# Kernel optimization log

Hardware: AMD Instinct MI355X
Metric: run time of the kernel (lower is better)

The kernel has to match this reference:

```python
import jax, jax.numpy as jnp
import numpy as np

EPS = 1e-5  # torch GroupNorm default eps


def _pairwise_sqdist(x, y):
    # squared euclidean distance matrix, clamped at 0 for numerical safety
    d = (jnp.sum(x * x, -1)[:, None] + jnp.sum(y * y, -1)[None, :]
         - 2.0 * (x @ y.T))
    return jnp.maximum(d, 0.0)


def _pc_normalize(ref, src):
    # jointly center and scale both clouds to the unit sphere
    pts = jnp.concatenate([ref, src], axis=0)
    centroid = pts.mean(axis=0, keepdims=True)
    pts = pts - centroid
    m = jnp.max(jnp.linalg.norm(pts, axis=1))
    pts = pts / m
    n_ref = ref.shape[0]
    return pts[:n_ref], pts[n_ref:]


def _group_norm(x, gamma, beta, groups):
    N, C = x.shape
    xg = x.reshape(N, groups, C // groups)
    mean = xg.mean(-1, keepdims=True)
    var = jnp.mean((xg - mean) ** 2, -1, keepdims=True)
    xn = ((xg - mean) / jnp.sqrt(var + EPS)).reshape(N, C)
    return xn * gamma + beta


def setup_inputs() -> dict:
    key = jax.random.key(0)
    ks = jax.random.split(key, 8)
    N_ref, N_src, D = 128, 128, 256
    points_c = jax.random.normal(ks[0], (N_ref + N_src, 3), jnp.float32)
    ref_feats = jax.random.normal(ks[1], (N_ref, D), jnp.float32)
    src_feats = jax.random.normal(ks[2], (N_src, D), jnp.float32)
    # normalized features, as the '_norm' names suggest
    ref_feats = ref_feats / jnp.linalg.norm(ref_feats, axis=-1, keepdims=True)
    src_feats = src_feats / jnp.linalg.norm(src_feats, axis=-1, keepdims=True)
    # a valid rigid transform: random rotation + small translation
    A = jax.random.normal(ks[3], (3, 3), jnp.float32)
    Q, _ = jnp.linalg.qr(A)
    trans = jnp.eye(4, dtype=jnp.float32)
    trans = trans.at[:3, :3].set(Q)
    trans = trans.at[:3, 3].set(jax.random.normal(ks[4], (3,), jnp.float32) * 0.1)
    s = 1.0 / np.sqrt(512)
    return {
        'points_c': points_c,
        'ref_feats_c_norm': ref_feats,
        'src_feats_c_norm': src_feats,
        'trans': trans,
        'W1': jax.random.normal(ks[5], (256, 512), jnp.float32) * s,
        'b1': jnp.zeros((256,), jnp.float32),
        'g1': jnp.ones((256,), jnp.float32),
        'bt1': jnp.zeros((256,), jnp.float32),
        'W2': jax.random.normal(ks[6], (128, 256), jnp.float32) * (1.0 / np.sqrt(256)),
        'b2': jnp.zeros((128,), jnp.float32),
        'g2': jnp.ones((128,), jnp.float32),
        'bt2': jnp.zeros((128,), jnp.float32),
        'W3': jax.random.normal(ks[7], (2, 128), jnp.float32) * (1.0 / np.sqrt(128)),
        'b3': jnp.zeros((2,), jnp.float32),
        'ref_length': 128,
    }


def reference(points_c, ref_feats_c_norm, src_feats_c_norm, trans,
              W1, b1, g1, bt1, W2, b2, g2, bt2, W3, b3, ref_length):
    GROUPS = 8
    ref_points = points_c[:ref_length]
    src_points = points_c[ref_length:]
    # apply rigid transform to src points
    src_points = src_points @ trans[:3, :3].T + trans[:3, 3]
    ref_n, src_n = _pc_normalize(ref_points, src_points)

    dist_mat = jnp.exp(-_pairwise_sqdist(ref_n, src_n))  # [Nr, Ns]
    match_idx_ref = jnp.argmax(dist_mat, axis=1)
    match_idx_src = jnp.argmax(dist_mat, axis=0)
    min_dist_ref = jnp.max(dist_mat, axis=1)
    min_dist_src = jnp.max(dist_mat, axis=0)

    feat_score_mat = ref_feats_c_norm @ src_feats_c_norm.T  # [Nr, Ns]
    feat_match_idx_ref = jnp.argmax(feat_score_mat, axis=1)
    feat_match_idx_src = jnp.argmax(feat_score_mat, axis=0)
    feat_match_ref = jnp.max(feat_score_mat, axis=1)
    feat_match_src = jnp.max(feat_score_mat, axis=0)

    r_idx = jnp.arange(feat_score_mat.shape[0])
    c_idx = jnp.arange(feat_score_mat.shape[1])
    feat_score_ref = feat_score_mat[r_idx, match_idx_ref]
    feat_score_src = feat_score_mat[match_idx_src, c_idx]
    dist_ref = dist_mat[r_idx, feat_match_idx_ref]
    dist_src = dist_mat[feat_match_idx_src, c_idx]

    min_dist = jnp.concatenate([min_dist_ref, min_dist_src])
    feat_score = jnp.concatenate([feat_score_ref, feat_score_src])
    perm_d = jnp.argsort(-min_dist)  # descending sort
    d_m = min_dist[perm_d] * feat_score[perm_d]

    match_feat = jnp.concatenate([feat_match_ref, feat_match_src])
    match_dist = jnp.concatenate([dist_ref, dist_src])
    perm_f = jnp.argsort(-match_feat)
    m_d = match_dist[perm_f] * match_feat[perm_f]

    geo_out = jnp.concatenate([d_m, m_d])[None, :]  # [1, 512]

    h = _group_norm(geo_out @ W1.T + b1, g1, bt1, GROUPS)
    h = jax.nn.relu(h)
    h = _group_norm(h @ W2.T + b2, g2, bt2, GROUPS)
    h = jax.nn.relu(h)
    return h @ W3.T + b3  # [1, num_classes]
```

## Files before the change

kernel.cpp:

```cpp
#include <hip/hip_runtime.h>
#include <math.h>

#define NREF 128
#define NSRC 128
#define DIM  256
#define EPS  1e-5f

__global__ __launch_bounds__(512) void feat_kernel(
    const float* __restrict__ ref_feats,
    const float* __restrict__ src_feats,
    const float* __restrict__ points_c,
    const float* __restrict__ trans,
    float* __restrict__ feat_mat,
    float* __restrict__ rowF, int* __restrict__ rowFi,
    float* __restrict__ pts_ws)
{
    __shared__ __align__(16) float refrow[DIM];
    __shared__ float wmv[8];  __shared__ int wmi[8];
    __shared__ float wred[16], red[4];

    const int t = threadIdx.x;
    const int w = t >> 6, l = t & 63;

    if (blockIdx.x == 128) {
        float x = 0.f, y = 0.f, z = 0.f;
        if (t < 256) {
            x = points_c[3 * t + 0];
            y = points_c[3 * t + 1];
            z = points_c[3 * t + 2];
            if (t >= NREF) {
                float nx = trans[0] * x + trans[1] * y + trans[2]  * z + trans[3];
                float ny = trans[4] * x + trans[5] * y + trans[6]  * z + trans[7];
                float nz = trans[8] * x + trans[9] * y + trans[10] * z + trans[11];
                x = nx; y = ny; z = nz;
            }
            float sx = x, sy = y, sz = z;
            for (int off = 32; off >= 1; off >>= 1) {
                sx += __shfl_down(sx, off);
                sy += __shfl_down(sy, off);
                sz += __shfl_down(sz, off);
            }
            if (l == 0) {
                wred[w] = sx; wred[4 + w] = sy; wred[8 + w] = sz;
            }
        }
        __syncthreads();
        if (t == 0) {
            red[0] = (wred[0] + wred[1] + wred[2] + wred[3]) * (1.0f / 256.0f);
            red[1] = (wred[4] + wred[5] + wred[6] + wred[7]) * (1.0f / 256.0f);
            red[2] = (wred[8] + wred[9] + wred[10] + wred[11]) * (1.0f / 256.0f);
        }
        __syncthreads();
        if (t < 256) {
            x -= red[0]; y -= red[1]; z -= red[2];
            float n = x * x + y * y + z * z;
            float mx = n;
            for (int off = 32; off >= 1; off >>= 1)
                mx = fmaxf(mx, __shfl_down(mx, off));
            if (l == 0) wred[w] = mx;
        }
        __syncthreads();
        if (t == 0)
            red[3] = 1.0f / sqrtf(fmaxf(fmaxf(wred[0], wred[1]), fmaxf(wred[2], wred[3])));
        __syncthreads();
        if (t < 256) {
            const float inv = red[3];
            x *= inv; y *= inv; z *= inv;
            pts_ws[t]       = x;
            pts_ws[256 + t] = y;
            pts_ws[512 + t] = z;
            pts_ws[768 + t] = x * x + y * y + z * z;
        }
        return;
    }

    const int i = blockIdx.x;
    if (t < 64) ((float4*)refrow)[t] = ((const float4*)(ref_feats + i * DIM))[t];
    __syncthreads();

    const float4 r = ((const float4*)refrow)[l];
    float bv = -2.f; int bi = 0;

    for (int m = 0; m < 16; m += 2) {
        const int j0 = w * 16 + m;
        const int j1 = j0 + 1;
        const float4 a0 = ((const float4*)(src_feats + j0 * DIM))[l];
        const float4 a1 = ((const float4*)(src_feats + j1 * DIM))[l];
        float acc0 = a0.x * r.x + a0.y * r.y + a0.z * r.z + a0.w * r.w;
        float acc1 = a1.x * r.x + a1.y * r.y + a1.z * r.z + a1.w * r.w;
        for (int off = 32; off >= 1; off >>= 1) {
            acc0 += __shfl_down(acc0, off);
            acc1 += __shfl_down(acc1, off);
        }
        if (l == 0) {
            feat_mat[i * NSRC + j0] = acc0;
            feat_mat[i * NSRC + j1] = acc1;
            if (acc0 > bv) { bv = acc0; bi = j0; }
            if (acc1 > bv) { bv = acc1; bi = j1; }
        }
    }
    if (l == 0) { wmv[w] = bv; wmi[w] = bi; }
    __syncthreads();
    if (t == 0) {
        float fv = -2.f; int fi = 0;
        for (int ww = 0; ww < 8; ++ww)
            if (wmv[ww] > fv) { fv = wmv[ww]; fi = wmi[ww]; }
        rowF[i] = fv; rowFi[i] = fi;
    }
}

__global__ __launch_bounds__(1024) void geo_kernel(
    const float* __restrict__ pts_ws,
    const float* __restrict__ feat_mat,
    const float* __restrict__ rowF, const int* __restrict__ rowFi,
    float* __restrict__ geo_out)
{
    __shared__ float px[256], py[256], pz[256], nsq[256];
    __shared__ float pvD[1024]; __shared__ int piD[1024];
    __shared__ float pvF[512];  __shared__ int piF[512];
    __shared__ float min_dist[256];   __shared__ int match_idx[256];
    __shared__ float match_feat[256]; __shared__ int feat_idx[256];
    __shared__ float feat_score[256], match_dist[256];
    __shared__ int prD[1024]; __shared__ int prF[1024];

    const int t = threadIdx.x;
    if (t < 256) {
        px[t]  = pts_ws[t];
        py[t]  = pts_ws[256 + t];
        pz[t]  = pts_ws[512 + t];
        nsq[t] = pts_ws[768 + t];
    }
    __syncthreads();

    {
        const int rc = t & 255, q = t >> 8;
        if (rc < 128) {
            const int i = rc;
            float bdv = -1.f; int bdi = 0;
            for (int m = 0; m < 32; ++m) {
                const int j = q * 32 + m;
                float d = nsq[i] + nsq[128 + j]
                        - 2.0f * (px[i] * px[128 + j] + py[i] * py[128 + j] + pz[i] * pz[128 + j]);
                d = fmaxf(d, 0.f);
                const float v = expf(-d);
                if (v > bdv) { bdv = v; bdi = j; }
            }
            pvD[q * 256 + rc] = bdv; piD[q * 256 + rc] = bdi;
        } else {
            const int j = rc - 128;
            float bdv = -1.f; int bdi = 0;
            float bfv = -2.f; int bfi = 0;
            for (int m = 0; m < 32; ++m) {
                const int i = q * 32 + m;
                float d = nsq[i] + nsq[128 + j]
                        - 2.0f * (px[i] * px[128 + j] + py[i] * py[128 + j] + pz[i] * pz[128 + j]);
                d = fmaxf(d, 0.f);
                const float v = expf(-d);
                if (v > bdv) { bdv = v; bdi = i; }
                const float f = feat_mat[i * NSRC + j];
                if (f > bfv) { bfv = f; bfi = i; }
            }
            pvD[q * 256 + rc] = bdv; piD[q * 256 + rc] = bdi;
            pvF[q * 128 + j]  = bfv; piF[q * 128 + j]  = bfi;
        }
    }
    __syncthreads();

    if (t < 256) {
        float bv = -1.f; int bi = 0;
        for (int q = 0; q < 4; ++q) {
            const float v = pvD[q * 256 + t];
            if (v > bv) { bv = v; bi = piD[q * 256 + t]; }
        }
        min_dist[t] = bv; match_idx[t] = bi;
        if (t < 128) {
            match_feat[t] = rowF[t]; feat_idx[t] = rowFi[t];
        } else {
            const int j = t - 128;
            float fv = -2.f; int fi = 0;
            for (int q = 0; q < 4; ++q) {
                const float v = pvF[q * 128 + j];
                if (v > fv) { fv = v; fi = piF[q * 128 + j]; }
            }
            match_feat[t] = fv; feat_idx[t] = fi;
        }
    }
    __syncthreads();

    if (t < 256) {
        if (t < NREF) {
            const int i = t;
            feat_score[t] = feat_mat[i * NSRC + match_idx[t]];
            const int j = feat_idx[t];
            float d = nsq[i] + nsq[128 + j]
                    - 2.0f * (px[i] * px[128 + j] + py[i] * py[128 + j] + pz[i] * pz[128 + j]);
            d = fmaxf(d, 0.f);
            match_dist[t] = expf(-d);
        } else {
            const int j = t - 128;
            feat_score[t] = feat_mat[match_idx[t] * NSRC + j];
            const int i = feat_idx[t];
            float d = nsq[i] + nsq[128 + j]
                    - 2.0f * (px[i] * px[128 + j] + py[i] * py[128 + j] + pz[i] * pz[128 + j]);
            d = fmaxf(d, 0.f);
            match_dist[t] = expf(-d);
        }
    }
    __syncthreads();

    {
        const int e = t & 255, q = t >> 8;
        const float v  = min_dist[e];
        const float wv = match_feat[e];
        int r1 = 0, r2 = 0;
        for (int m = 0; m < 64; ++m) {
            const int j = q * 64 + m;
            const float u  = min_dist[j];
            r1 += (u > v) || (u == v && j < e);
            const float uf = match_feat[j];
            r2 += (uf > wv) || (uf == wv && j < e);
        }
        prD[q * 256 + e] = r1;
        prF[q * 256 + e] = r2;
    }
    __syncthreads();
    if (t < 256) {
        const int r  = prD[t] + prD[256 + t] + prD[512 + t] + prD[768 + t];
        geo_out[r] = min_dist[t] * feat_score[t];
        const int rf = prF[t] + prF[256 + t] + prF[512 + t] + prF[768 + t];
        geo_out[256 + rf] = match_dist[t] * match_feat[t];
    }
}

__global__ __launch_bounds__(64) void mlp1_kernel(
    const float* __restrict__ geo,
    const float* __restrict__ W1, const float* __restrict__ b1,
    float* __restrict__ y1)
{
    const int c = blockIdx.x, l = threadIdx.x;
    const float4 ga = ((const float4*)geo)[l];
    const float4 gb = ((const float4*)geo)[64 + l];
    const float4* __restrict__ wrow = (const float4*)(W1 + c * 512);
    const float4 a = wrow[l];
    const float4 b = wrow[64 + l];
    float acc = a.x * ga.x + a.y * ga.y + a.z * ga.z + a.w * ga.w
              + b.x * gb.x + b.y * gb.y + b.z * gb.z + b.w * gb.w;
    acc += __shfl_down(acc, 32);
    acc += __shfl_down(acc, 16);
    acc += __shfl_down(acc, 8);
    acc += __shfl_down(acc, 4);
    acc += __shfl_down(acc, 2);
    acc += __shfl_down(acc, 1);
    if (l == 0) y1[c] = acc + b1[c];
}

__global__ __launch_bounds__(64) void mlp2_kernel(
    const float* __restrict__ y1,
    const float* __restrict__ g1, const float* __restrict__ bt1,
    const float* __restrict__ W2, const float* __restrict__ b2,
    float* __restrict__ y2)
{
    __shared__ __align__(16) float y1s[256];
    __shared__ float stats[16];
    const int c = blockIdx.x, l = threadIdx.x;
    ((float4*)y1s)[l] = ((const float4*)y1)[l];
    __syncthreads();
    if (l < 8) {
        float s = 0.f;
        for (int k = 0; k < 32; ++k) s += y1s[(l << 5) + k];
        const float mean = s * (1.0f / 32.0f);
        float q = 0.f;
        for (int k = 0; k < 32; ++k) { const float d = y1s[(l << 5) + k] - mean; q += d * d; }
        const float var = q * (1.0f / 32.0f);
        stats[l] = mean;
        stats[8 + l] = rsqrtf(var + EPS);
    }
    __syncthreads();
    const float4 gg = ((const float4*)g1)[l];
    const float4 bb = ((const float4*)bt1)[l];
    const int g = l >> 3;
    const float mean = stats[g], inv = stats[8 + g];
    const float4 yv = ((const float4*)y1s)[l];
    float4 h;
    h.x = fmaxf((yv.x - mean) * inv * gg.x + bb.x, 0.f);
    h.y = fmaxf((yv.y - mean) * inv * gg.y + bb.y, 0.f);
    h.z = fmaxf((yv.z - mean) * inv * gg.z + bb.z, 0.f);
    h.w = fmaxf((yv.w - mean) * inv * gg.w + bb.w, 0.f);
    const float4 wv = ((const float4*)(W2 + c * 256))[l];
    float acc = wv.x * h.x + wv.y * h.y + wv.z * h.z + wv.w * h.w;
    acc += __shfl_down(acc, 32);
    acc += __shfl_down(acc, 16);
    acc += __shfl_down(acc, 8);
    acc += __shfl_down(acc, 4);
    acc += __shfl_down(acc, 2);
    acc += __shfl_down(acc, 1);
    if (l == 0) y2[c] = acc + b2[c];
}

__global__ __launch_bounds__(128) void final_kernel(
    const float* __restrict__ y2,
    const float* __restrict__ g2, const float* __restrict__ bt2,
    const float* __restrict__ W3, const float* __restrict__ b3,
    float* __restrict__ out)
{
    __shared__ float y2s[128], h2[128];
    const int t = threadIdx.x;
    y2s[t] = y2[t];
    __syncthreads();
    {
        const int g = t >> 4;
        float s = 0.f;
        for (int k = 0; k < 16; ++k) s += y2s[(g << 4) + k];
        const float mean = s * (1.0f / 16.0f);
        float q = 0.f;
        for (int k = 0; k < 16; ++k) { const float d = y2s[(g << 4) + k] - mean; q += d * d; }
        const float var = q * (1.0f / 16.0f);
        const float xn = (y2s[t] - mean) * rsqrtf(var + EPS);
        h2[t] = fmaxf(xn * g2[t] + bt2[t], 0.f);
    }
    __syncthreads();
    const int wave = t >> 6, lane = t & 63;
    float acc = W3[wave * 128 + lane] * h2[lane]
              + W3[wave * 128 + 64 + lane] * h2[64 + lane];
    acc += __shfl_down(acc, 32);
    acc += __shfl_down(acc, 16);
    acc += __shfl_down(acc, 8);
    acc += __shfl_down(acc, 4);
    acc += __shfl_down(acc, 2);
    acc += __shfl_down(acc, 1);
    if (lane == 0) out[wave] = acc + b3[wave];
}

extern "C" void kernel_launch(void* const* d_in, const int* in_sizes, int n_in,
                              void* d_out, int out_size, void* d_ws, size_t ws_size,
                              hipStream_t stream)
{
    const float* points_c  = (const float*)d_in[0];
    const float* ref_feats = (const float*)d_in[1];
    const float* src_feats = (const float*)d_in[2];
    const float* trans     = (const float*)d_in[3];
    const float* W1  = (const float*)d_in[4];
    const float* b1  = (const float*)d_in[5];
    const float* g1  = (const float*)d_in[6];
    const float* bt1 = (const float*)d_in[7];
    const float* W2  = (const float*)d_in[8];
    const float* b2  = (const float*)d_in[9];
    const float* g2  = (const float*)d_in[10];
    const float* bt2 = (const float*)d_in[11];
    const float* W3  = (const float*)d_in[12];
    const float* b3  = (const float*)d_in[13];

    float* base     = (float*)d_ws;
    float* feat_mat = base;
    float* rowF     = base + 16384;
    int*   rowFi    = (int*)(base + 16512);
    float* pts_ws   = base + 16640;
    float* geo      = base + 17664;
    float* y1       = base + 18176;
    float* y2       = base + 18432;

    feat_kernel<<<dim3(129), dim3(512), 0, stream>>>(
        ref_feats, src_feats, points_c, trans, feat_mat, rowF, rowFi, pts_ws);
    geo_kernel<<<dim3(1), dim3(1024), 0, stream>>>(pts_ws, feat_mat, rowF, rowFi, geo);
    mlp1_kernel<<<dim3(256), dim3(64), 0, stream>>>(geo, W1, b1, y1);
    mlp2_kernel<<<dim3(128), dim3(64), 0, stream>>>(y1, g1, bt1, W2, b2, y2);
    final_kernel<<<dim3(1), dim3(128), 0, stream>>>(y2, g2, bt2, W3, b3, (float*)d_out);
}
```

Baseline: 107.2 us.

## Fuse geo and final kernels into predecessors via last-block atomic counter

Merges geo_kernel into feat_kernel using a last-block-done pattern: every block increments an atomic counter and the final block runs the geometry/sorting stage with 512 threads instead of 1024. Likewise final_kernel is folded into mlp2_kernel's last block. This drops two kernel launches and their launch gaps, but adds a memset launch, threadfences and atomics, and halves the parallelism of the geometry stage, which now runs serially after the last arriving block.

Measured after the change: 130.7 us. 1.22x slower.

```diff
diff --git a/kernel.cpp b/kernel.cpp
--- a/kernel.cpp
+++ b/kernel.cpp
@@ -6,18 +6,28 @@
 #define DIM  256
 #define EPS  1e-5f
 
-__global__ __launch_bounds__(512) void feat_kernel(
+__global__ __launch_bounds__(512) void front_kernel(
     const float* __restrict__ ref_feats,
     const float* __restrict__ src_feats,
     const float* __restrict__ points_c,
     const float* __restrict__ trans,
     float* __restrict__ feat_mat,
     float* __restrict__ rowF, int* __restrict__ rowFi,
-    float* __restrict__ pts_ws)
+    float* __restrict__ pts_ws,
+    float* __restrict__ geo_out,
+    int* __restrict__ counter)
 {
     __shared__ __align__(16) float refrow[DIM];
     __shared__ float wmv[8];  __shared__ int wmi[8];
     __shared__ float wred[16], red[4];
+    __shared__ float px[256], py[256], pz[256], nsq[256];
+    __shared__ float pvD[512]; __shared__ int piD[512];
+    __shared__ float pvF[256]; __shared__ int piF[256];
+    __shared__ float min_dist[256];   __shared__ int match_idx[256];
+    __shared__ float match_feat[256]; __shared__ int feat_idx[256];
+    __shared__ float feat_score[256], match_dist[256];
+    __shared__ int prD[512]; __shared__ int prF[512];
+    __shared__ int is_last;
 
     const int t = threadIdx.x;
     const int w = t >> 6, l = t & 63;
@@ -40,9 +50,7 @@
                 sy += __shfl_down(sy, off);
                 sz += __shfl_down(sz, off);
             }
-            if (l == 0) {
-                wred[w] = sx; wred[4 + w] = sy; wred[8 + w] = sz;
-            }
+            if (l == 0) { wred[w] = sx; wred[4 + w] = sy; wred[8 + w] = sz; }
         }
         __syncthreads();
         if (t == 0) {
@@ -71,59 +79,49 @@
             pts_ws[512 + t] = z;
             pts_ws[768 + t] = x * x + y * y + z * z;
         }
-        return;
-    }
-
-    const int i = blockIdx.x;
-    if (t < 64) ((float4*)refrow)[t] = ((const float4*)(ref_feats + i * DIM))[t];
-    __syncthreads();
-
-    const float4 r = ((const float4*)refrow)[l];
-    float bv = -2.f; int bi = 0;
-
-    for (int m = 0; m < 16; m += 2) {
-        const int j0 = w * 16 + m;
-        const int j1 = j0 + 1;
-        const float4 a0 = ((const float4*)(src_feats + j0 * DIM))[l];
-        const float4 a1 = ((const float4*)(src_feats + j1 * DIM))[l];
-        float acc0 = a0.x * r.x + a0.y * r.y + a0.z * r.z + a0.w * r.w;
-        float acc1 = a1.x * r.x + a1.y * r.y + a1.z * r.z + a1.w * r.w;
-        for (int off = 32; off >= 1; off >>= 1) {
-            acc0 += __shfl_down(acc0, off);
-            acc1 += __shfl_down(acc1, off);
-        }
-        if (l == 0) {
-            feat_mat[i * NSRC + j0] = acc0;
-            feat_mat[i * NSRC + j1] = acc1;
-            if (acc0 > bv) { bv = acc0; bi = j0; }
-            if (acc1 > bv) { bv = acc1; bi = j1; }
-        }
-    }
-    if (l == 0) { wmv[w] = bv; wmi[w] = bi; }
-    __syncthreads();
-    if (t == 0) {
-        float fv = -2.f; int fi = 0;
-        for (int ww = 0; ww < 8; ++ww)
-            if (wmv[ww] > fv) { fv = wmv[ww]; fi = wmi[ww]; }
-        rowF[i] = fv; rowFi[i] = fi;
-    }
-}
-
-__global__ __launch_bounds__(1024) void geo_kernel(
-    const float* __restrict__ pts_ws,
-    const float* __restrict__ feat_mat,
-    const float* __restrict__ rowF, const int* __restrict__ rowFi,
-    float* __restrict__ geo_out)
-{
-    __shared__ float px[256], py[256], pz[256], nsq[256];
-    __shared__ float pvD[1024]; __shared__ int piD[1024];
-    __shared__ float pvF[512];  __shared__ int piF[512];
-    __shared__ float min_dist[256];   __shared__ int match_idx[256];
-    __shared__ float match_feat[256]; __shared__ int feat_idx[256];
-    __shared__ float feat_score[256], match_dist[256];
-    __shared__ int prD[1024]; __shared__ int prF[1024];
-
-    const int t = threadIdx.x;
+    } else {
+        const int i = blockIdx.x;
+        if (t < 64) ((float4*)refrow)[t] = ((const float4*)(ref_feats + i * DIM))[t];
+        __syncthreads();
+
+        const float4 r = ((const float4*)refrow)[l];
+        float bv = -2.f; int bi = 0;
+
+        for (int m = 0; m < 16; m += 2) {
+            const int j0 = w * 16 + m;
+            const int j1 = j0 + 1;
+            const float4 a0 = ((const float4*)(src_feats + j0 * DIM))[l];
+            const float4 a1 = ((const float4*)(src_feats + j1 * DIM))[l];
+            float acc0 = a0.x * r.x + a0.y * r.y + a0.z * r.z + a0.w * r.w;
+            float acc1 = a1.x * r.x + a1.y * r.y + a1.z * r.z + a1.w * r.w;
+            for (int off = 32; off >= 1; off >>= 1) {
+                acc0 += __shfl_down(acc0, off);
+                acc1 += __shfl_down(acc1, off);
+            }
+            if (l == 0) {
+                feat_mat[i * NSRC + j0] = acc0;
+                feat_mat[i * NSRC + j1] = acc1;
+                if (acc0 > bv) { bv = acc0; bi = j0; }
+                if (acc1 > bv) { bv = acc1; bi = j1; }
+            }
+        }
+        if (l == 0) { wmv[w] = bv; wmi[w] = bi; }
+        __syncthreads();
+        if (t == 0) {
+            float fv = -2.f; int fi = 0;
+            for (int ww = 0; ww < 8; ++ww)
+                if (wmv[ww] > fv) { fv = wmv[ww]; fi = wmi[ww]; }
+            rowF[i] = fv; rowFi[i] = fi;
+        }
+    }
+
+    __syncthreads();
+    __threadfence();
+    if (t == 0) is_last = (atomicAdd(counter, 1) == 128);
+    __syncthreads();
+    if (!is_last) return;
+    __threadfence();
+
     if (t < 256) {
         px[t]  = pts_ws[t];
         py[t]  = pts_ws[256 + t];
@@ -137,8 +135,8 @@
         if (rc < 128) {
             const int i = rc;
             float bdv = -1.f; int bdi = 0;
-            for (int m = 0; m < 32; ++m) {
-                const int j = q * 32 + m;
+            for (int m = 0; m < 64; ++m) {
+                const int j = q * 64 + m;
                 float d = nsq[i] + nsq[128 + j]
                         - 2.0f * (px[i] * px[128 + j] + py[i] * py[128 + j] + pz[i] * pz[128 + j]);
                 d = fmaxf(d, 0.f);
@@ -150,8 +148,8 @@
             const int j = rc - 128;
             float bdv = -1.f; int bdi = 0;
             float bfv = -2.f; int bfi = 0;
-            for (int m = 0; m < 32; ++m) {
-                const int i = q * 32 + m;
+            for (int m = 0; m < 64; ++m) {
+                const int i = q * 64 + m;
                 float d = nsq[i] + nsq[128 + j]
                         - 2.0f * (px[i] * px[128 + j] + py[i] * py[128 + j] + pz[i] * pz[128 + j]);
                 d = fmaxf(d, 0.f);
@@ -168,7 +166,7 @@
 
     if (t < 256) {
         float bv = -1.f; int bi = 0;
-        for (int q = 0; q < 4; ++q) {
+        for (int q = 0; q < 2; ++q) {
             const float v = pvD[q * 256 + t];
             if (v > bv) { bv = v; bi = piD[q * 256 + t]; }
         }
@@ -178,7 +176,7 @@
         } else {
             const int j = t - 128;
             float fv = -2.f; int fi = 0;
-            for (int q = 0; q < 4; ++q) {
+            for (int q = 0; q < 2; ++q) {
                 const float v = pvF[q * 128 + j];
                 if (v > fv) { fv = v; fi = piF[q * 128 + j]; }
             }
@@ -213,8 +211,8 @@
         const float v  = min_dist[e];
         const float wv = match_feat[e];
         int r1 = 0, r2 = 0;
-        for (int m = 0; m < 64; ++m) {
-            const int j = q * 64 + m;
+        for (int m = 0; m < 128; ++m) {
+            const int j = q * 128 + m;
             const float u  = min_dist[j];
             r1 += (u > v) || (u == v && j < e);
             const float uf = match_feat[j];
@@ -225,9 +223,9 @@
     }
     __syncthreads();
     if (t < 256) {
-        const int r  = prD[t] + prD[256 + t] + prD[512 + t] + prD[768 + t];
+        const int r  = prD[t] + prD[256 + t];
         geo_out[r] = min_dist[t] * feat_score[t];
-        const int rf = prF[t] + prF[256 + t] + prF[512 + t] + prF[768 + t];
+        const int rf = prF[t] + prF[256 + t];
         geo_out[256 + rf] = match_dist[t] * match_feat[t];
     }
 }
@@ -258,10 +256,16 @@
     const float* __restrict__ y1,
     const float* __restrict__ g1, const float* __restrict__ bt1,
     const float* __restrict__ W2, const float* __restrict__ b2,
-    float* __restrict__ y2)
+    const float* __restrict__ g2, const float* __restrict__ bt2,
+    const float* __restrict__ W3, const float* __restrict__ b3,
+    float* __restrict__ y2,
+    float* __restrict__ out,
+    int* __restrict__ counter)
 {
     __shared__ __align__(16) float y1s[256];
     __shared__ float stats[16];
+    __shared__ float y2s[128], h2s[128];
+    __shared__ int is_last;
     const int c = blockIdx.x, l = threadIdx.x;
     ((float4*)y1s)[l] = ((const float4*)y1)[l];
     __syncthreads();
@@ -276,59 +280,60 @@
         stats[8 + l] = rsqrtf(var + EPS);
     }
     __syncthreads();
-    const float4 gg = ((const float4*)g1)[l];
-    const float4 bb = ((const float4*)bt1)[l];
-    const int g = l >> 3;
-    const float mean = stats[g], inv = stats[8 + g];
-    const float4 yv = ((const float4*)y1s)[l];
-    float4 h;
-    h.x = fmaxf((yv.x - mean) * inv * gg.x + bb.x, 0.f);
-    h.y = fmaxf((yv.y - mean) * inv * gg.y + bb.y, 0.f);
-    h.z = fmaxf((yv.z - mean) * inv * gg.z + bb.z, 0.f);
-    h.w = fmaxf((yv.w - mean) * inv * gg.w + bb.w, 0.f);
-    const float4 wv = ((const float4*)(W2 + c * 256))[l];
-    float acc = wv.x * h.x + wv.y * h.y + wv.z * h.z + wv.w * h.w;
-    acc += __shfl_down(acc, 32);
-    acc += __shfl_down(acc, 16);
-    acc += __shfl_down(acc, 8);
-    acc += __shfl_down(acc, 4);
-    acc += __shfl_down(acc, 2);
-    acc += __shfl_down(acc, 1);
-    if (l == 0) y2[c] = acc + b2[c];
-}
-
-__global__ __launch_bounds__(128) void final_kernel(
-    const float* __restrict__ y2,
-    const float* __restrict__ g2, const float* __restrict__ bt2,
-    const float* __restrict__ W3, const float* __restrict__ b3,
-    float* __restrict__ out)
-{
-    __shared__ float y2s[128], h2[128];
-    const int t = threadIdx.x;
-    y2s[t] = y2[t];
-    __syncthreads();
     {
-        const int g = t >> 4;
+        const float4 gg = ((const float4*)g1)[l];
+        const float4 bb = ((const float4*)bt1)[l];
+        const int g = l >> 3;
+        const float mean = stats[g], inv = stats[8 + g];
+        const float4 yv = ((const float4*)y1s)[l];
+        float4 h;
+        h.x = fmaxf((yv.x - mean) * inv * gg.x + bb.x, 0.f);
+        h.y = fmaxf((yv.y - mean) * inv * gg.y + bb.y, 0.f);
+        h.z = fmaxf((yv.z - mean) * inv * gg.z + bb.z, 0.f);
+        h.w = fmaxf((yv.w - mean) * inv * gg.w + bb.w, 0.f);
+        const float4 wv = ((const float4*)(W2 + c * 256))[l];
+        float acc = wv.x * h.x + wv.y * h.y + wv.z * h.z + wv.w * h.w;
+        acc += __shfl_down(acc, 32);
+        acc += __shfl_down(acc, 16);
+        acc += __shfl_down(acc, 8);
+        acc += __shfl_down(acc, 4);
+        acc += __shfl_down(acc, 2);
+        acc += __shfl_down(acc, 1);
+        if (l == 0) y2[c] = acc + b2[c];
+    }
+
+    __threadfence();
+    if (l == 0) is_last = (atomicAdd(counter, 1) == 127);
+    __syncthreads();
+    if (!is_last) return;
+    __threadfence();
+
+    y2s[l]      = y2[l];
+    y2s[64 + l] = y2[64 + l];
+    __syncthreads();
+    for (int cc = l; cc < 128; cc += 64) {
+        const int g = cc >> 4;
         float s = 0.f;
         for (int k = 0; k < 16; ++k) s += y2s[(g << 4) + k];
         const float mean = s * (1.0f / 16.0f);
         float q = 0.f;
         for (int k = 0; k < 16; ++k) { const float d = y2s[(g << 4) + k] - mean; q += d * d; }
         const float var = q * (1.0f / 16.0f);
-        const float xn = (y2s[t] - mean) * rsqrtf(var + EPS);
-        h2[t] = fmaxf(xn * g2[t] + bt2[t], 0.f);
-    }
-    __syncthreads();
-    const int wave = t >> 6, lane = t & 63;
-    float acc = W3[wave * 128 + lane] * h2[lane]
-              + W3[wave * 128 + 64 + lane] * h2[64 + lane];
-    acc += __shfl_down(acc, 32);
-    acc += __shfl_down(acc, 16);
-    acc += __shfl_down(acc, 8);
-    acc += __shfl_down(acc, 4);
-    acc += __shfl_down(acc, 2);
-    acc += __shfl_down(acc, 1);
-    if (lane == 0) out[wave] = acc + b3[wave];
+        const float xn = (y2s[cc] - mean) * rsqrtf(var + EPS);
+        h2s[cc] = fmaxf(xn * g2[cc] + bt2[cc], 0.f);
+    }
+    __syncthreads();
+    for (int o = 0; o < 2; ++o) {
+        float acc = W3[o * 128 + l] * h2s[l]
+                  + W3[o * 128 + 64 + l] * h2s[64 + l];
+        acc += __shfl_down(acc, 32);
+        acc += __shfl_down(acc, 16);
+        acc += __shfl_down(acc, 8);
+        acc += __shfl_down(acc, 4);
+        acc += __shfl_down(acc, 2);
+        acc += __shfl_down(acc, 1);
+        if (l == 0) out[o] = acc + b3[o];
+    }
 }
 
 extern "C" void kernel_launch(void* const* d_in, const int* in_sizes, int n_in,
@@ -358,11 +363,13 @@
     float* geo      = base + 17664;
     float* y1       = base + 18176;
     float* y2       = base + 18432;
-
-    feat_kernel<<<dim3(129), dim3(512), 0, stream>>>(
-        ref_feats, src_feats, points_c, trans, feat_mat, rowF, rowFi, pts_ws);
-    geo_kernel<<<dim3(1), dim3(1024), 0, stream>>>(pts_ws, feat_mat, rowF, rowFi, geo);
+    int*   counters = (int*)(base + 18560);
+
+    hipMemsetAsync(counters, 0, 2 * sizeof(int), stream);
+    front_kernel<<<dim3(129), dim3(512), 0, stream>>>(
+        ref_feats, src_feats, points_c, trans,
+        feat_mat, rowF, rowFi, pts_ws, geo, counters);
     mlp1_kernel<<<dim3(256), dim3(64), 0, stream>>>(geo, W1, b1, y1);
-    mlp2_kernel<<<dim3(128), dim3(64), 0, stream>>>(y1, g1, bt1, W2, b2, y2);
-    final_kernel<<<dim3(1), dim3(128), 0, stream>>>(y2, g2, bt2, W3, b3, (float*)d_out);
+    mlp2_kernel<<<dim3(128), dim3(64), 0, stream>>>(
+        y1, g1, bt1, W2, b2, g2, bt2, W3, b3, y2, (float*)d_out, counters + 1);
 }
```

## Compute column argmax via packed atomics and fuse final MLP into last block

Applied to the files above, without the earlier changes.

The feature kernel now computes all 16 dot products per wave with unrolled independent loads and xor-shuffle reductions. It writes the results with float4 stores and publishes per-column maxima through 64-bit packed atomicMax, with ties broken toward the lower row index. This removes the strided column scan of feat_mat from the single-block geo kernel. The final group-norm/linear stage is folded into mlp2 through a last-block-done counter, which removes one launch. The cost is an extra memset and 16K global atomics.

After: 132.0 us. 23.1% more time.

```diff
diff --git a/kernel.cpp b/kernel.cpp
--- a/kernel.cpp
+++ b/kernel.cpp
@@ -13,6 +13,7 @@
     const float* __restrict__ trans,
     float* __restrict__ feat_mat,
     float* __restrict__ rowF, int* __restrict__ rowFi,
+    unsigned long long* __restrict__ colmax,
     float* __restrict__ pts_ws)
 {
     __shared__ __align__(16) float refrow[DIM];
@@ -40,9 +41,7 @@
                 sy += __shfl_down(sy, off);
                 sz += __shfl_down(sz, off);
             }
-            if (l == 0) {
-                wred[w] = sx; wred[4 + w] = sy; wred[8 + w] = sz;
-            }
+            if (l == 0) { wred[w] = sx; wred[4 + w] = sy; wred[8 + w] = sz; }
         }
         __syncthreads();
         if (t == 0) {
@@ -79,27 +78,50 @@
     __syncthreads();
 
     const float4 r = ((const float4*)refrow)[l];
-    float bv = -2.f; int bi = 0;
-
-    for (int m = 0; m < 16; m += 2) {
-        const int j0 = w * 16 + m;
-        const int j1 = j0 + 1;
-        const float4 a0 = ((const float4*)(src_feats + j0 * DIM))[l];
-        const float4 a1 = ((const float4*)(src_feats + j1 * DIM))[l];
-        float acc0 = a0.x * r.x + a0.y * r.y + a0.z * r.z + a0.w * r.w;
-        float acc1 = a1.x * r.x + a1.y * r.y + a1.z * r.z + a1.w * r.w;
-        for (int off = 32; off >= 1; off >>= 1) {
-            acc0 += __shfl_down(acc0, off);
-            acc1 += __shfl_down(acc1, off);
-        }
-        if (l == 0) {
-            feat_mat[i * NSRC + j0] = acc0;
-            feat_mat[i * NSRC + j1] = acc1;
-            if (acc0 > bv) { bv = acc0; bi = j0; }
-            if (acc1 > bv) { bv = acc1; bi = j1; }
-        }
-    }
-    if (l == 0) { wmv[w] = bv; wmi[w] = bi; }
+
+    float dot[16];
+#pragma unroll
+    for (int m = 0; m < 16; ++m) {
+        const float4 a = ((const float4*)(src_feats + (w * 16 + m) * DIM))[l];
+        dot[m] = a.x * r.x + a.y * r.y + a.z * r.z + a.w * r.w;
+    }
+#pragma unroll
+    for (int m = 0; m < 16; ++m) {
+        float s = dot[m];
+        s += __shfl_xor(s, 32);
+        s += __shfl_xor(s, 16);
+        s += __shfl_xor(s, 8);
+        s += __shfl_xor(s, 4);
+        s += __shfl_xor(s, 2);
+        s += __shfl_xor(s, 1);
+        dot[m] = s;
+    }
+
+    if (l == 0) {
+        const int j0 = w * 16;
+        float4 v;
+        v.x = dot[0];  v.y = dot[1];  v.z = dot[2];  v.w = dot[3];
+        ((float4*)(feat_mat + i * NSRC + j0))[0] = v;
+        v.x = dot[4];  v.y = dot[5];  v.z = dot[6];  v.w = dot[7];
+        ((float4*)(feat_mat + i * NSRC + j0))[1] = v;
+        v.x = dot[8];  v.y = dot[9];  v.z = dot[10]; v.w = dot[11];
+        ((float4*)(feat_mat + i * NSRC + j0))[2] = v;
+        v.x = dot[12]; v.y = dot[13]; v.z = dot[14]; v.w = dot[15];
+        ((float4*)(feat_mat + i * NSRC + j0))[3] = v;
+
+        float bv = -2.f; int bi = 0;
+#pragma unroll
+        for (int m = 0; m < 16; ++m) {
+            const int j = j0 + m;
+            const unsigned int b   = __float_as_uint(dot[m]);
+            const unsigned int key = (b & 0x80000000u) ? ~b : (b | 0x80000000u);
+            const unsigned long long packed =
+                ((unsigned long long)key << 32) | (unsigned int)(127 - i);
+            atomicMax(&colmax[j], packed);
+            if (dot[m] > bv) { bv = dot[m]; bi = j; }
+        }
+        wmv[w] = bv; wmi[w] = bi;
+    }
     __syncthreads();
     if (t == 0) {
         float fv = -2.f; int fi = 0;
@@ -113,11 +135,11 @@
     const float* __restrict__ pts_ws,
     const float* __restrict__ feat_mat,
     const float* __restrict__ rowF, const int* __restrict__ rowFi,
+    const unsigned long long* __restrict__ colmax,
     float* __restrict__ geo_out)
 {
     __shared__ float px[256], py[256], pz[256], nsq[256];
     __shared__ float pvD[1024]; __shared__ int piD[1024];
-    __shared__ float pvF[512];  __shared__ int piF[512];
     __shared__ float min_dist[256];   __shared__ int match_idx[256];
     __shared__ float match_feat[256]; __shared__ int feat_idx[256];
     __shared__ float feat_score[256], match_dist[256];
@@ -134,9 +156,9 @@
 
     {
         const int rc = t & 255, q = t >> 8;
+        float bdv = -1.f; int bdi = 0;
         if (rc < 128) {
             const int i = rc;
-            float bdv = -1.f; int bdi = 0;
             for (int m = 0; m < 32; ++m) {
                 const int j = q * 32 + m;
                 float d = nsq[i] + nsq[128 + j]
@@ -145,11 +167,8 @@
                 const float v = expf(-d);
                 if (v > bdv) { bdv = v; bdi = j; }
             }
-            pvD[q * 256 + rc] = bdv; piD[q * 256 + rc] = bdi;
         } else {
             const int j = rc - 128;
-            float bdv = -1.f; int bdi = 0;
-            float bfv = -2.f; int bfi = 0;
             for (int m = 0; m < 32; ++m) {
                 const int i = q * 32 + m;
                 float d = nsq[i] + nsq[128 + j]
@@ -157,12 +176,9 @@
                 d = fmaxf(d, 0.f);
                 const float v = expf(-d);
                 if (v > bdv) { bdv = v; bdi = i; }
-                const float f = feat_mat[i * NSRC + j];
-                if (f > bfv) { bfv = f; bfi = i; }
             }
-            pvD[q * 256 + rc] = bdv; piD[q * 256 + rc] = bdi;
-            pvF[q * 128 + j]  = bfv; piF[q * 128 + j]  = bfi;
-        }
+        }
+        pvD[q * 256 + rc] = bdv; piD[q * 256 + rc] = bdi;
     }
     __syncthreads();
 
@@ -176,13 +192,11 @@
         if (t < 128) {
             match_feat[t] = rowF[t]; feat_idx[t] = rowFi[t];
         } else {
-            const int j = t - 128;
-            float fv = -2.f; int fi = 0;
-            for (int q = 0; q < 4; ++q) {
-                const float v = pvF[q * 128 + j];
-                if (v > fv) { fv = v; fi = piF[q * 128 + j]; }
-            }
-            match_feat[t] = fv; feat_idx[t] = fi;
+            const unsigned long long p = colmax[t - 128];
+            const unsigned int key = (unsigned int)(p >> 32);
+            const unsigned int fb  = (key & 0x80000000u) ? (key & 0x7FFFFFFFu) : ~key;
+            match_feat[t] = __uint_as_float(fb);
+            feat_idx[t]   = 127 - (int)(p & 0xFFFFFFFFu);
         }
     }
     __syncthreads();
@@ -258,10 +272,16 @@
     const float* __restrict__ y1,
     const float* __restrict__ g1, const float* __restrict__ bt1,
     const float* __restrict__ W2, const float* __restrict__ b2,
-    float* __restrict__ y2)
+    const float* __restrict__ g2, const float* __restrict__ bt2,
+    const float* __restrict__ W3, const float* __restrict__ b3,
+    float* __restrict__ y2,
+    float* __restrict__ out,
+    int* __restrict__ counter)
 {
     __shared__ __align__(16) float y1s[256];
     __shared__ float stats[16];
+    __shared__ float y2s[128], h2s[128];
+    __shared__ int is_last;
     const int c = blockIdx.x, l = threadIdx.x;
     ((float4*)y1s)[l] = ((const float4*)y1)[l];
     __syncthreads();
@@ -276,59 +296,60 @@
         stats[8 + l] = rsqrtf(var + EPS);
     }
     __syncthreads();
-    const float4 gg = ((const float4*)g1)[l];
-    const float4 bb = ((const float4*)bt1)[l];
-    const int g = l >> 3;
-    const float mean = stats[g], inv = stats[8 + g];
-    const float4 yv = ((const float4*)y1s)[l];
-    float4 h;
-    h.x = fmaxf((yv.x - mean) * inv * gg.x + bb.x, 0.f);
-    h.y = fmaxf((yv.y - mean) * inv * gg.y + bb.y, 0.f);
-    h.z = fmaxf((yv.z - mean) * inv * gg.z + bb.z, 0.f);
-    h.w = fmaxf((yv.w - mean) * inv * gg.w + bb.w, 0.f);
-    const float4 wv = ((const float4*)(W2 + c * 256))[l];
-    float acc = wv.x * h.x + wv.y * h.y + wv.z * h.z + wv.w * h.w;
-    acc += __shfl_down(acc, 32);
-    acc += __shfl_down(acc, 16);
-    acc += __shfl_down(acc, 8);
-    acc += __shfl_down(acc, 4);
-    acc += __shfl_down(acc, 2);
-    acc += __shfl_down(acc, 1);
-    if (l == 0) y2[c] = acc + b2[c];
-}
-
-__global__ __launch_bounds__(128) void final_kernel(
-    const float* __restrict__ y2,
-    const float* __restrict__ g2, const float* __restrict__ bt2,
-    const float* __restrict__ W3, const float* __restrict__ b3,
-    float* __restrict__ out)
-{
-    __shared__ float y2s[128], h2[128];
-    const int t = threadIdx.x;
-    y2s[t] = y2[t];
-    __syncthreads();
     {
-        const int g = t >> 4;
+        const float4 gg = ((const float4*)g1)[l];
+        const float4 bb = ((const float4*)bt1)[l];
+        const int g = l >> 3;
+        const float mean = stats[g], inv = stats[8 + g];
+        const float4 yv = ((const float4*)y1s)[l];
+        float4 h;
+        h.x = fmaxf((yv.x - mean) * inv * gg.x + bb.x, 0.f);
+        h.y = fmaxf((yv.y - mean) * inv * gg.y + bb.y, 0.f);
+        h.z = fmaxf((yv.z - mean) * inv * gg.z + bb.z, 0.f);
+        h.w = fmaxf((yv.w - mean) * inv * gg.w + bb.w, 0.f);
+        const float4 wv = ((const float4*)(W2 + c * 256))[l];
+        float acc = wv.x * h.x + wv.y * h.y + wv.z * h.z + wv.w * h.w;
+        acc += __shfl_down(acc, 32);
+        acc += __shfl_down(acc, 16);
+        acc += __shfl_down(acc, 8);
+        acc += __shfl_down(acc, 4);
+        acc += __shfl_down(acc, 2);
+        acc += __shfl_down(acc, 1);
+        if (l == 0) y2[c] = acc + b2[c];
+    }
+
+    __threadfence();
+    if (l == 0) is_last = (atomicAdd(counter, 1) == 127);
+    __syncthreads();
+    if (!is_last) return;
+    __threadfence();
+
+    y2s[l]      = y2[l];
+    y2s[64 + l] = y2[64 + l];
+    __syncthreads();
+    for (int cc = l; cc < 128; cc += 64) {
+        const int g = cc >> 4;
         float s = 0.f;
         for (int k = 0; k < 16; ++k) s += y2s[(g << 4) + k];
         const float mean = s * (1.0f / 16.0f);
         float q = 0.f;
         for (int k = 0; k < 16; ++k) { const float d = y2s[(g << 4) + k] - mean; q += d * d; }
         const float var = q * (1.0f / 16.0f);
-        const float xn = (y2s[t] - mean) * rsqrtf(var + EPS);
-        h2[t] = fmaxf(xn * g2[t] + bt2[t], 0.f);
-    }
-    __syncthreads();
-    const int wave = t >> 6, lane = t & 63;
-    float acc = W3[wave * 128 + lane] * h2[lane]
-              + W3[wave * 128 + 64 + lane] * h2[64 + lane];
-    acc += __shfl_down(acc, 32);
-    acc += __shfl_down(acc, 16);
-    acc += __shfl_down(acc, 8);
-    acc += __shfl_down(acc, 4);
-    acc += __shfl_down(acc, 2);
-    acc += __shfl_down(acc, 1);
-    if (lane == 0) out[wave] = acc + b3[wave];
+        const float xn = (y2s[cc] - mean) * rsqrtf(var + EPS);
+        h2s[cc] = fmaxf(xn * g2[cc] + bt2[cc], 0.f);
+    }
+    __syncthreads();
+    for (int o = 0; o < 2; ++o) {
+        float acc = W3[o * 128 + l] * h2s[l]
+                  + W3[o * 128 + 64 + l] * h2s[64 + l];
+        acc += __shfl_down(acc, 32);
+        acc += __shfl_down(acc, 16);
+        acc += __shfl_down(acc, 8);
+        acc += __shfl_down(acc, 4);
+        acc += __shfl_down(acc, 2);
+        acc += __shfl_down(acc, 1);
+        if (l == 0) out[o] = acc + b3[o];
+    }
 }
 
 extern "C" void kernel_launch(void* const* d_in, const int* in_sizes, int n_in,
@@ -358,11 +379,17 @@
     float* geo      = base + 17664;
     float* y1       = base + 18176;
     float* y2       = base + 18432;
+    unsigned long long* colmax = (unsigned long long*)(base + 18560);
+    int*   counter  = (int*)(base + 18816);
+
+    hipMemsetAsync(colmax, 0, 128 * sizeof(unsigned long long) + sizeof(int), stream);
 
     feat_kernel<<<dim3(129), dim3(512), 0, stream>>>(
-        ref_feats, src_feats, points_c, trans, feat_mat, rowF, rowFi, pts_ws);
-    geo_kernel<<<dim3(1), dim3(1024), 0, stream>>>(pts_ws, feat_mat, rowF, rowFi, geo);
+        ref_feats, src_feats, points_c, trans,
+        feat_mat, rowF, rowFi, colmax, pts_ws);
+    geo_kernel<<<dim3(1), dim3(1024), 0, stream>>>(
+        pts_ws, feat_mat, rowF, rowFi, colmax, geo);
     mlp1_kernel<<<dim3(256), dim3(64), 0, stream>>>(geo, W1, b1, y1);
-    mlp2_kernel<<<dim3(128), dim3(64), 0, stream>>>(y1, g1, bt1, W2, b2, y2);
-    final_kernel<<<dim3(1), dim3(128), 0, stream>>>(y2, g2, bt2, W3, b3, (float*)d_out);
-}
+    mlp2_kernel<<<dim3(128), dim3(64), 0, stream>>>(
+        y1, g1, bt1, W2, b2, g2, bt2, W3, b3, y2, (float*)d_out, counter);
+}
```

## Move point normalization into geo kernel and batch feature dot products

Applied to the files above, without the earlier changes.

Point-cloud centering and scaling moves out of a special extra block in feat_kernel and into the single-block geo_kernel, which writes the results straight to shared memory instead of a global workspace. feat_kernel now issues all 16 row loads up front, reduces each with xor shuffles, and writes results as float4 stores. geo_kernel also preloads its feat_mat column values into registers and unrolls its loops. This adds latency-bound serial reduction work to the single-block geo kernel in exchange for a global round-trip and more load-level parallelism in feat_kernel, at the cost of higher register pressure.

Result: no change. 106.4 us (-0.8%).

```diff
diff --git a/kernel.cpp b/kernel.cpp
--- a/kernel.cpp
+++ b/kernel.cpp
@@ -9,97 +9,57 @@
 __global__ __launch_bounds__(512) void feat_kernel(
     const float* __restrict__ ref_feats,
     const float* __restrict__ src_feats,
-    const float* __restrict__ points_c,
-    const float* __restrict__ trans,
     float* __restrict__ feat_mat,
-    float* __restrict__ rowF, int* __restrict__ rowFi,
-    float* __restrict__ pts_ws)
+    float* __restrict__ rowF, int* __restrict__ rowFi)
 {
     __shared__ __align__(16) float refrow[DIM];
     __shared__ float wmv[8];  __shared__ int wmi[8];
-    __shared__ float wred[16], red[4];
 
     const int t = threadIdx.x;
     const int w = t >> 6, l = t & 63;
-
-    if (blockIdx.x == 128) {
-        float x = 0.f, y = 0.f, z = 0.f;
-        if (t < 256) {
-            x = points_c[3 * t + 0];
-            y = points_c[3 * t + 1];
-            z = points_c[3 * t + 2];
-            if (t >= NREF) {
-                float nx = trans[0] * x + trans[1] * y + trans[2]  * z + trans[3];
-                float ny = trans[4] * x + trans[5] * y + trans[6]  * z + trans[7];
-                float nz = trans[8] * x + trans[9] * y + trans[10] * z + trans[11];
-                x = nx; y = ny; z = nz;
-            }
-            float sx = x, sy = y, sz = z;
-            for (int off = 32; off >= 1; off >>= 1) {
-                sx += __shfl_down(sx, off);
-                sy += __shfl_down(sy, off);
-                sz += __shfl_down(sz, off);
-            }
-            if (l == 0) {
-                wred[w] = sx; wred[4 + w] = sy; wred[8 + w] = sz;
-            }
-        }
-        __syncthreads();
-        if (t == 0) {
-            red[0] = (wred[0] + wred[1] + wred[2] + wred[3]) * (1.0f / 256.0f);
-            red[1] = (wred[4] + wred[5] + wred[6] + wred[7]) * (1.0f / 256.0f);
-            red[2] = (wred[8] + wred[9] + wred[10] + wred[11]) * (1.0f / 256.0f);
-        }
-        __syncthreads();
-        if (t < 256) {
-            x -= red[0]; y -= red[1]; z -= red[2];
-            float n = x * x + y * y + z * z;
-            float mx = n;
-            for (int off = 32; off >= 1; off >>= 1)
-                mx = fmaxf(mx, __shfl_down(mx, off));
-            if (l == 0) wred[w] = mx;
-        }
-        __syncthreads();
-        if (t == 0)
-            red[3] = 1.0f / sqrtf(fmaxf(fmaxf(wred[0], wred[1]), fmaxf(wred[2], wred[3])));
-        __syncthreads();
-        if (t < 256) {
-            const float inv = red[3];
-            x *= inv; y *= inv; z *= inv;
-            pts_ws[t]       = x;
-            pts_ws[256 + t] = y;
-            pts_ws[512 + t] = z;
-            pts_ws[768 + t] = x * x + y * y + z * z;
-        }
-        return;
-    }
-
     const int i = blockIdx.x;
+
     if (t < 64) ((float4*)refrow)[t] = ((const float4*)(ref_feats + i * DIM))[t];
     __syncthreads();
 
     const float4 r = ((const float4*)refrow)[l];
-    float bv = -2.f; int bi = 0;
-
-    for (int m = 0; m < 16; m += 2) {
-        const int j0 = w * 16 + m;
-        const int j1 = j0 + 1;
-        const float4 a0 = ((const float4*)(src_feats + j0 * DIM))[l];
-        const float4 a1 = ((const float4*)(src_feats + j1 * DIM))[l];
-        float acc0 = a0.x * r.x + a0.y * r.y + a0.z * r.z + a0.w * r.w;
-        float acc1 = a1.x * r.x + a1.y * r.y + a1.z * r.z + a1.w * r.w;
-        for (int off = 32; off >= 1; off >>= 1) {
-            acc0 += __shfl_down(acc0, off);
-            acc1 += __shfl_down(acc1, off);
-        }
-        if (l == 0) {
-            feat_mat[i * NSRC + j0] = acc0;
-            feat_mat[i * NSRC + j1] = acc1;
-            if (acc0 > bv) { bv = acc0; bi = j0; }
-            if (acc1 > bv) { bv = acc1; bi = j1; }
-        }
-    }
-    if (l == 0) { wmv[w] = bv; wmi[w] = bi; }
+
+    float dot[16];
+#pragma unroll
+    for (int m = 0; m < 16; ++m) {
+        const float4 a = ((const float4*)(src_feats + (w * 16 + m) * DIM))[l];
+        dot[m] = a.x * r.x + a.y * r.y + a.z * r.z + a.w * r.w;
+    }
+#pragma unroll
+    for (int m = 0; m < 16; ++m) {
+        float s = dot[m];
+        s += __shfl_xor(s, 32);
+        s += __shfl_xor(s, 16);
+        s += __shfl_xor(s, 8);
+        s += __shfl_xor(s, 4);
+        s += __shfl_xor(s, 2);
+        s += __shfl_xor(s, 1);
+        dot[m] = s;
+    }
+
+    if (l == 0) {
+        const int j0 = w * 16;
+        float4 v;
+        v.x = dot[0];  v.y = dot[1];  v.z = dot[2];  v.w = dot[3];
+        ((float4*)(feat_mat + i * NSRC + j0))[0] = v;
+        v.x = dot[4];  v.y = dot[5];  v.z = dot[6];  v.w = dot[7];
+        ((float4*)(feat_mat + i * NSRC + j0))[1] = v;
+        v.x = dot[8];  v.y = dot[9];  v.z = dot[10]; v.w = dot[11];
+        ((float4*)(feat_mat + i * NSRC + j0))[2] = v;
+        v.x = dot[12]; v.y = dot[13]; v.z = dot[14]; v.w = dot[15];
+        ((float4*)(feat_mat + i * NSRC + j0))[3] = v;
+
+        float bv = -2.f; int bi = 0;
+#pragma unroll
+        for (int m = 0; m < 16; ++m)
+            if (dot[m] > bv) { bv = dot[m]; bi = j0 + m; }
+        wmv[w] = bv; wmi[w] = bi;
+    }
     __syncthreads();
     if (t == 0) {
         float fv = -2.f; int fi = 0;
@@ -110,12 +70,14 @@
 }
 
 __global__ __launch_bounds__(1024) void geo_kernel(
-    const float* __restrict__ pts_ws,
+    const float* __restrict__ points_c,
+    const float* __restrict__ trans,
     const float* __restrict__ feat_mat,
     const float* __restrict__ rowF, const int* __restrict__ rowFi,
     float* __restrict__ geo_out)
 {
     __shared__ float px[256], py[256], pz[256], nsq[256];
+    __shared__ float wred[16], red[4];
     __shared__ float pvD[1024]; __shared__ int piD[1024];
     __shared__ float pvF[512];  __shared__ int piF[512];
     __shared__ float min_dist[256];   __shared__ int match_idx[256];
@@ -123,12 +85,54 @@
     __shared__ float feat_score[256], match_dist[256];
     __shared__ int prD[1024]; __shared__ int prF[1024];
 
-    const int t = threadIdx.x;
-    if (t < 256) {
-        px[t]  = pts_ws[t];
-        py[t]  = pts_ws[256 + t];
-        pz[t]  = pts_ws[512 + t];
-        nsq[t] = pts_ws[768 + t];
+    const int t    = threadIdx.x;
+    const int wave = t >> 6;
+    const int lane = t & 63;
+
+    float x = 0.f, y = 0.f, z = 0.f;
+    if (t < 256) {
+        x = points_c[3 * t + 0];
+        y = points_c[3 * t + 1];
+        z = points_c[3 * t + 2];
+        if (t >= NREF) {
+            float nx = trans[0] * x + trans[1] * y + trans[2]  * z + trans[3];
+            float ny = trans[4] * x + trans[5] * y + trans[6]  * z + trans[7];
+            float nz = trans[8] * x + trans[9] * y + trans[10] * z + trans[11];
+            x = nx; y = ny; z = nz;
+        }
+        float sx = x, sy = y, sz = z;
+        for (int off = 32; off >= 1; off >>= 1) {
+            sx += __shfl_down(sx, off);
+            sy += __shfl_down(sy, off);
+            sz += __shfl_down(sz, off);
+        }
+        if (lane == 0) { wred[wave] = sx; wred[4 + wave] = sy; wred[8 + wave] = sz; }
+    }
+    __syncthreads();
+    if (t == 0) {
+        red[0] = (wred[0] + wred[1] + wred[2] + wred[3]) * (1.0f / 256.0f);
+        red[1] = (wred[4] + wred[5] + wred[6] + wred[7]) * (1.0f / 256.0f);
+        red[2] = (wred[8] + wred[9] + wred[10] + wred[11]) * (1.0f / 256.0f);
+    }
+    __syncthreads();
+
+    if (t < 256) {
+        x -= red[0]; y -= red[1]; z -= red[2];
+        float n = x * x + y * y + z * z;
+        float mx = n;
+        for (int off = 32; off >= 1; off >>= 1)
+            mx = fmaxf(mx, __shfl_down(mx, off));
+        if (lane == 0) wred[wave] = mx;
+    }
+    __syncthreads();
+    if (t == 0)
+        red[3] = 1.0f / sqrtf(fmaxf(fmaxf(wred[0], wred[1]), fmaxf(wred[2], wred[3])));
+    __syncthreads();
+    if (t < 256) {
+        const float inv = red[3];
+        x *= inv; y *= inv; z *= inv;
+        px[t] = x; py[t] = y; pz[t] = z;
+        nsq[t] = x * x + y * y + z * z;
     }
     __syncthreads();
 
@@ -137,6 +141,7 @@
         if (rc < 128) {
             const int i = rc;
             float bdv = -1.f; int bdi = 0;
+#pragma unroll
             for (int m = 0; m < 32; ++m) {
                 const int j = q * 32 + m;
                 float d = nsq[i] + nsq[128 + j]
@@ -148,8 +153,13 @@
             pvD[q * 256 + rc] = bdv; piD[q * 256 + rc] = bdi;
         } else {
             const int j = rc - 128;
+            float f[32];
+#pragma unroll
+            for (int m = 0; m < 32; ++m)
+                f[m] = feat_mat[(q * 32 + m) * NSRC + j];
             float bdv = -1.f; int bdi = 0;
             float bfv = -2.f; int bfi = 0;
+#pragma unroll
             for (int m = 0; m < 32; ++m) {
                 const int i = q * 32 + m;
                 float d = nsq[i] + nsq[128 + j]
@@ -157,8 +167,7 @@
                 d = fmaxf(d, 0.f);
                 const float v = expf(-d);
                 if (v > bdv) { bdv = v; bdi = i; }
-                const float f = feat_mat[i * NSRC + j];
-                if (f > bfv) { bfv = f; bfi = i; }
+                if (f[m] > bfv) { bfv = f[m]; bfi = i; }
             }
             pvD[q * 256 + rc] = bdv; piD[q * 256 + rc] = bdi;
             pvF[q * 128 + j]  = bfv; piF[q * 128 + j]  = bfi;
@@ -354,14 +363,14 @@
     float* feat_mat = base;
     float* rowF     = base + 16384;
     int*   rowFi    = (int*)(base + 16512);
-    float* pts_ws   = base + 16640;
-    float* geo      = base + 17664;
-    float* y1       = base + 18176;
-    float* y2       = base + 18432;
-
-    feat_kernel<<<dim3(129), dim3(512), 0, stream>>>(
-        ref_feats, src_feats, points_c, trans, feat_mat, rowF, rowFi, pts_ws);
-    geo_kernel<<<dim3(1), dim3(1024), 0, stream>>>(pts_ws, feat_mat, rowF, rowFi, geo);
+    float* geo      = base + 16640;
+    float* y1       = base + 17152;
+    float* y2       = base + 17408;
+
+    feat_kernel<<<dim3(128), dim3(512), 0, stream>>>(
+        ref_feats, src_feats, feat_mat, rowF, rowFi);
+    geo_kernel<<<dim3(1), dim3(1024), 0, stream>>>(
+        points_c, trans, feat_mat, rowF, rowFi, geo);
     mlp1_kernel<<<dim3(256), dim3(64), 0, stream>>>(geo, W1, b1, y1);
     mlp2_kernel<<<dim3(128), dim3(64), 0, stream>>>(y1, g1, bt1, W2, b2, y2);
     final_kernel<<<dim3(1), dim3(128), 0, stream>>>(y2, g2, bt2, W3, b3, (float*)d_out);
```
